# Kernel optimization log

Measured on AMD Instinct MI355X. Metric: run time of the kernel, lower is better.

Reference implementation:

```python
import jax, jax.numpy as jnp
import numpy as np

N = 100000
D_FEAT = 256
HID = 128
EMB = 64
FANOUT = 16


def setup_inputs() -> dict:
    key = jax.random.key(0)
    k = jax.random.split(key, 7)
    s = 0.05
    features = jax.random.normal(k[0], (N, D_FEAT), dtype=jnp.float32)
    W1 = jax.random.normal(k[1], (HID, 2 * D_FEAT), dtype=jnp.float32) * s
    W2 = jax.random.normal(k[2], (HID, 2 * HID), dtype=jnp.float32) * s
    W3 = jax.random.normal(k[3], (HID, 2 * HID), dtype=jnp.float32) * s
    W4 = jax.random.normal(k[4], (EMB, 2 * HID), dtype=jnp.float32) * s
    nodes = jnp.arange(N, dtype=jnp.int32)
    neigh = jax.random.randint(k[5], (N, FANOUT), 0, N, dtype=jnp.int32)
    return {"features": features, "W1": W1, "W2": W2, "W3": W3, "W4": W4,
            "nodes": nodes, "neigh": neigh}


def _sage_layer(h, neigh, W):
    # MeanAggregator: mean of sampled neighbor features  [N, d]
    neigh_mean = jnp.mean(h[neigh], axis=1)
    # Encoder (gcn=False): relu(W @ cat([self, neigh_mean]).T) -> [N, out]
    combined = jnp.concatenate([h, neigh_mean], axis=1)  # [N, 2d]
    return jax.nn.relu(combined @ W.T)


def reference(features, W1, W2, W3, W4, nodes, neigh):
    h1 = _sage_layer(features, neigh, W1)  # [N, HID]
    h2 = _sage_layer(h1, neigh, W2)        # [N, HID]
    h3 = _sage_layer(h2, neigh, W3)        # [N, HID]
    h4 = _sage_layer(h3, neigh, W4)        # [N, EMB]
    # GraphEmbeddingModule.forward returns gSAGE4(n).t() -> [len(n), EMB]
    return h4[nodes]
```

## Files before the change

### kernel.cpp

```cpp
#include <hip/hip_runtime.h>
#include <hip/hip_bf16.h>


constexpr int N_NODES = 100000;
constexpr int FANOUT  = 16;

typedef __attribute__((ext_vector_type(8))) short short8;
typedef __attribute__((ext_vector_type(4))) float f32x4;

__device__ inline unsigned short bf16_rne(float f) {
    unsigned u = __float_as_uint(f);
    return (unsigned short)((u + 0x7fffu + ((u >> 16) & 1u)) >> 16);
}
__device__ inline float bf16_tof(unsigned short s) {
    return __uint_as_float(((unsigned)s) << 16);
}

__global__ __launch_bounds__(256)
void prep_Bck(const float* __restrict__ W, unsigned short* __restrict__ Bhi,
              unsigned short* __restrict__ Blo, int D_IN, int D_OUT)
{
    int i = blockIdx.x * 256 + threadIdx.x;
    int total = 2 * D_OUT * D_IN;
    if (i >= total) return;
    int c = i / D_IN, k = i % D_IN;
    float v = (c < D_OUT) ? W[(size_t)c * (2 * D_IN) + k]
                          : W[(size_t)(c - D_OUT) * (2 * D_IN) + D_IN + k];
    unsigned short hi = bf16_rne(v);
    Bhi[i] = hi;
    Blo[i] = bf16_rne(v - bf16_tof(hi));
}

__global__ __launch_bounds__(256, 3)
void gemm1(const float* __restrict__ hf,
           const unsigned short* __restrict__ Bhi,
           const unsigned short* __restrict__ Blo,
           float* __restrict__ gs, unsigned short* __restrict__ gn, int N)
{
    constexpr int K = 256, C = 256, DO = 128, LDA = 40, LDB = 40;
    __shared__ unsigned short Ah[64 * LDA], Al[64 * LDA];
    __shared__ unsigned short Bh[C * LDB], Bl[C * LDB];

    const int tid  = threadIdx.x;
    const int wave = tid >> 6;
    const int lane = tid & 63;
    const int ml   = lane & 15;
    const int quad = lane >> 4;
    const int node0 = blockIdx.x * 64;

    f32x4 acc[4][4];
    #pragma unroll
    for (int mi = 0; mi < 4; ++mi)
        #pragma unroll
        for (int ni = 0; ni < 4; ++ni)
            acc[mi][ni] = (f32x4){0.f, 0.f, 0.f, 0.f};

    for (int k0 = 0; k0 < K; k0 += 32) {
        #pragma unroll
        for (int t = 0; t < 2; ++t) {
            int idx = tid + t * 256;
            int row = idx >> 3, c4 = idx & 7;
            int nd = node0 + row; if (nd >= N) nd = N - 1;
            float4 v = *(const float4*)&hf[(size_t)nd * K + k0 + c4 * 4];
            float vv[4] = {v.x, v.y, v.z, v.w};
            unsigned short hi[4], lo[4];
            #pragma unroll
            for (int e = 0; e < 4; ++e) {
                hi[e] = bf16_rne(vv[e]);
                lo[e] = bf16_rne(vv[e] - bf16_tof(hi[e]));
            }
            *(uint2*)&Ah[row * LDA + c4 * 4] = *(const uint2*)hi;
            *(uint2*)&Al[row * LDA + c4 * 4] = *(const uint2*)lo;
        }
        #pragma unroll
        for (int t = 0; t < 8; ++t) {
            int idx = tid + t * 256;
            int pl  = idx >> 10;
            int rem = idx & 1023;
            int row = rem >> 2, ch = rem & 3;
            const unsigned short* src = (pl ? Blo : Bhi) + (size_t)row * K + k0 + ch * 8;
            unsigned short* dst = (pl ? Bl : Bh) + row * LDB + ch * 8;
            *(uint4*)dst = *(const uint4*)src;
        }
        __syncthreads();

        short8 afh[4], afl[4];
        #pragma unroll
        for (int mi = 0; mi < 4; ++mi) {
            int r = mi * 16 + ml;
            afh[mi] = *(const short8*)&Ah[r * LDA + quad * 8];
            afl[mi] = *(const short8*)&Al[r * LDA + quad * 8];
        }
        #pragma unroll
        for (int ni = 0; ni < 4; ++ni) {
            int c = wave * 64 + ni * 16 + ml;
            short8 bh = *(const short8*)&Bh[c * LDB + quad * 8];
            short8 bl = *(const short8*)&Bl[c * LDB + quad * 8];
            #pragma unroll
            for (int mi = 0; mi < 4; ++mi) {
                acc[mi][ni] = __builtin_amdgcn_mfma_f32_16x16x32_bf16(afl[mi], bh, acc[mi][ni], 0, 0, 0);
                acc[mi][ni] = __builtin_amdgcn_mfma_f32_16x16x32_bf16(afh[mi], bl, acc[mi][ni], 0, 0, 0);
                acc[mi][ni] = __builtin_amdgcn_mfma_f32_16x16x32_bf16(afh[mi], bh, acc[mi][ni], 0, 0, 0);
            }
        }
        __syncthreads();
    }

    #pragma unroll
    for (int mi = 0; mi < 4; ++mi)
        #pragma unroll
        for (int r = 0; r < 4; ++r) {
            int node = node0 + mi * 16 + quad * 4 + r;
            if (node >= N) continue;
            #pragma unroll
            for (int ni = 0; ni < 4; ++ni) {
                int c = wave * 64 + ni * 16 + ml;
                float v = acc[mi][ni][r];
                if (c < DO) gs[(size_t)node * DO + c] = v;
                else        gn[(size_t)node * DO + (c - DO)] = bf16_rne(v);
            }
        }
}

template<int C>
__global__ __launch_bounds__(256, 2)
void fused_layer(const float* __restrict__ gs_in,
                 const unsigned short* __restrict__ gn_in,
                 const int* __restrict__ neigh,
                 const unsigned short* __restrict__ Bhi,
                 const unsigned short* __restrict__ Blo,
                 float* __restrict__ gs_out,
                 unsigned short* __restrict__ gn_out, int N)
{
    constexpr int K = 128, DO = C / 2, NI = C / 64, LDAF = 136, LDB = 40;
    __shared__ unsigned short Afh[64 * LDAF], Afl[64 * LDAF];
    __shared__ unsigned short Bh[C * LDB], Bl[C * LDB];

    const int tid  = threadIdx.x;
    const int wave = tid >> 6;
    const int lane = tid & 63;
    const int ml   = lane & 15;
    const int quad = lane >> 4;
    const int node0 = blockIdx.x * 64;

    {
        const int row = tid >> 2;
        const int seg = tid & 3;
        int nd = node0 + row; if (nd >= N) nd = N - 1;
        const int4* nb4 = (const int4*)(neigh + (size_t)nd * FANOUT);
        int4 q0 = nb4[0], q1 = nb4[1], q2 = nb4[2], q3 = nb4[3];
        int ids[FANOUT] = {q0.x, q0.y, q0.z, q0.w, q1.x, q1.y, q1.z, q1.w,
                           q2.x, q2.y, q2.z, q2.w, q3.x, q3.y, q3.z, q3.w};
        float acc[32];
        #pragma unroll
        for (int c = 0; c < 32; ++c) acc[c] = 0.f;
        #pragma unroll
        for (int j = 0; j < FANOUT; ++j) {
            const uint4* src = (const uint4*)&gn_in[(size_t)ids[j] * 128 + seg * 32];
            #pragma unroll
            for (int t = 0; t < 4; ++t) {
                uint4 q = src[t];
                acc[t*8+0] += __uint_as_float(q.x << 16);
                acc[t*8+1] += __uint_as_float(q.x & 0xffff0000u);
                acc[t*8+2] += __uint_as_float(q.y << 16);
                acc[t*8+3] += __uint_as_float(q.y & 0xffff0000u);
                acc[t*8+4] += __uint_as_float(q.z << 16);
                acc[t*8+5] += __uint_as_float(q.z & 0xffff0000u);
                acc[t*8+6] += __uint_as_float(q.w << 16);
                acc[t*8+7] += __uint_as_float(q.w & 0xffff0000u);
            }
        }
        const float inv = 1.0f / (float)FANOUT;
        alignas(16) unsigned short th[32], tl[32];
        const float4* gsp = (const float4*)&gs_in[(size_t)nd * 128 + seg * 32];
        #pragma unroll
        for (int t = 0; t < 8; ++t) {
            float4 s = gsp[t];
            float sv[4] = {s.x, s.y, s.z, s.w};
            #pragma unroll
            for (int e = 0; e < 4; ++e) {
                float h = fmaxf(fmaf(acc[t*4+e], inv, sv[e]), 0.f);
                unsigned short hi = bf16_rne(h);
                th[t*4+e] = hi;
                tl[t*4+e] = bf16_rne(h - bf16_tof(hi));
            }
        }
        #pragma unroll
        for (int t = 0; t < 4; ++t) {
            *(uint4*)&Afh[row * LDAF + seg * 32 + t * 8] = *(const uint4*)&th[t * 8];
            *(uint4*)&Afl[row * LDAF + seg * 32 + t * 8] = *(const uint4*)&tl[t * 8];
        }
    }

    f32x4 acc[4][NI];
    #pragma unroll
    for (int mi = 0; mi < 4; ++mi)
        #pragma unroll
        for (int ni = 0; ni < NI; ++ni)
            acc[mi][ni] = (f32x4){0.f, 0.f, 0.f, 0.f};

    for (int k0 = 0; k0 < K; k0 += 32) {
        constexpr int TOT = 2 * C * 4;
        #pragma unroll
        for (int t = 0; t < TOT / 256; ++t) {
            int idx = tid + t * 256;
            int pl  = idx / (C * 4);
            int rem = idx % (C * 4);
            int row = rem >> 2, ch = rem & 3;
            const unsigned short* src = (pl ? Blo : Bhi) + (size_t)row * K + k0 + ch * 8;
            unsigned short* dst = (pl ? Bl : Bh) + row * LDB + ch * 8;
            *(uint4*)dst = *(const uint4*)src;
        }
        __syncthreads();

        short8 afh[4], afl[4];
        #pragma unroll
        for (int mi = 0; mi < 4; ++mi) {
            int r = mi * 16 + ml;
            afh[mi] = *(const short8*)&Afh[r * LDAF + k0 + quad * 8];
            afl[mi] = *(const short8*)&Afl[r * LDAF + k0 + quad * 8];
        }
        #pragma unroll
        for (int ni = 0; ni < NI; ++ni) {
            int c = wave * (16 * NI) + ni * 16 + ml;
            short8 bh = *(const short8*)&Bh[c * LDB + quad * 8];
            short8 bl = *(const short8*)&Bl[c * LDB + quad * 8];
            #pragma unroll
            for (int mi = 0; mi < 4; ++mi) {
                acc[mi][ni] = __builtin_amdgcn_mfma_f32_16x16x32_bf16(afl[mi], bh, acc[mi][ni], 0, 0, 0);
                acc[mi][ni] = __builtin_amdgcn_mfma_f32_16x16x32_bf16(afh[mi], bl, acc[mi][ni], 0, 0, 0);
                acc[mi][ni] = __builtin_amdgcn_mfma_f32_16x16x32_bf16(afh[mi], bh, acc[mi][ni], 0, 0, 0);
            }
        }
        __syncthreads();
    }

    #pragma unroll
    for (int mi = 0; mi < 4; ++mi)
        #pragma unroll
        for (int r = 0; r < 4; ++r) {
            int node = node0 + mi * 16 + quad * 4 + r;
            if (node >= N) continue;
            #pragma unroll
            for (int ni = 0; ni < NI; ++ni) {
                int c = wave * (16 * NI) + ni * 16 + ml;
                float v = acc[mi][ni][r];
                if (c < DO) gs_out[(size_t)node * DO + c] = v;
                else        gn_out[(size_t)node * DO + (c - DO)] = bf16_rne(v);
            }
        }
}

__global__ __launch_bounds__(256)
void agg_out(const float* __restrict__ gs4, const unsigned short* __restrict__ gn4,
             const int* __restrict__ neigh, const int* __restrict__ nodes,
             float* __restrict__ out, int N)
{
    const int i    = blockIdx.x * 32 + (threadIdx.x >> 3);
    const int lane = threadIdx.x & 7;
    if (i >= N) return;
    const int nd = nodes[i];
    const int4* nb4 = (const int4*)(neigh + (size_t)nd * FANOUT);
    int4 q0 = nb4[0], q1 = nb4[1], q2 = nb4[2], q3 = nb4[3];
    int ids[FANOUT] = {q0.x, q0.y, q0.z, q0.w, q1.x, q1.y, q1.z, q1.w,
                       q2.x, q2.y, q2.z, q2.w, q3.x, q3.y, q3.z, q3.w};
    float acc[8];
    #pragma unroll
    for (int c = 0; c < 8; ++c) acc[c] = 0.f;
    #pragma unroll
    for (int j = 0; j < FANOUT; ++j) {
        uint4 q = *(const uint4*)&gn4[(size_t)ids[j] * 64 + lane * 8];
        acc[0] += __uint_as_float(q.x << 16);
        acc[1] += __uint_as_float(q.x & 0xffff0000u);
        acc[2] += __uint_as_float(q.y << 16);
        acc[3] += __uint_as_float(q.y & 0xffff0000u);
        acc[4] += __uint_as_float(q.z << 16);
        acc[5] += __uint_as_float(q.z & 0xffff0000u);
        acc[6] += __uint_as_float(q.w << 16);
        acc[7] += __uint_as_float(q.w & 0xffff0000u);
    }
    const float inv = 1.0f / (float)FANOUT;
    const float* s = gs4 + (size_t)nd * 64 + lane * 8;
    float4 s0 = *(const float4*)&s[0];
    float4 s1 = *(const float4*)&s[4];
    float4 o0, o1;
    o0.x = fmaxf(fmaf(acc[0], inv, s0.x), 0.f);
    o0.y = fmaxf(fmaf(acc[1], inv, s0.y), 0.f);
    o0.z = fmaxf(fmaf(acc[2], inv, s0.z), 0.f);
    o0.w = fmaxf(fmaf(acc[3], inv, s0.w), 0.f);
    o1.x = fmaxf(fmaf(acc[4], inv, s1.x), 0.f);
    o1.y = fmaxf(fmaf(acc[5], inv, s1.y), 0.f);
    o1.z = fmaxf(fmaf(acc[6], inv, s1.z), 0.f);
    o1.w = fmaxf(fmaf(acc[7], inv, s1.w), 0.f);
    float* op = out + (size_t)i * 64 + lane * 8;
    *(float4*)&op[0] = o0;
    *(float4*)&op[4] = o1;
}

extern "C" void kernel_launch(void* const* d_in, const int* in_sizes, int n_in,
                              void* d_out, int out_size, void* d_ws, size_t ws_size,
                              hipStream_t stream)
{
    const float* features = (const float*)d_in[0];
    const float* W1       = (const float*)d_in[1];
    const float* W2       = (const float*)d_in[2];
    const float* W3       = (const float*)d_in[3];
    const float* W4       = (const float*)d_in[4];
    const int*   nodes    = (const int*)d_in[5];
    const int*   neigh    = (const int*)d_in[6];
    float*       out      = (float*)d_out;

    unsigned short* B1h = (unsigned short*)d_ws;
    unsigned short* B1l = B1h + 65536;
    unsigned short* B2h = B1l + 65536;
    unsigned short* B2l = B2h + 32768;
    unsigned short* B3h = B2l + 32768;
    unsigned short* B3l = B3h + 32768;
    unsigned short* B4h = B3l + 32768;
    unsigned short* B4l = B4h + 16384;
    float* gs = (float*)(B4l + 16384);
    unsigned short* gnA = (unsigned short*)(gs + (size_t)N_NODES * 128);
    unsigned short* gnB = gnA + (size_t)N_NODES * 128;
    float* gs4 = (float*)gnB;
    unsigned short* gn4 = gnB + (size_t)N_NODES * 128;

    prep_Bck<<<(65536 + 255) / 256, 256, 0, stream>>>(W1, B1h, B1l, 256, 128);
    prep_Bck<<<(32768 + 255) / 256, 256, 0, stream>>>(W2, B2h, B2l, 128, 128);
    prep_Bck<<<(32768 + 255) / 256, 256, 0, stream>>>(W3, B3h, B3l, 128, 128);
    prep_Bck<<<(16384 + 255) / 256, 256, 0, stream>>>(W4, B4h, B4l, 128, 64);

    const int grid = (N_NODES + 63) / 64;

    gemm1<<<grid, 256, 0, stream>>>(features, B1h, B1l, gs, gnA, N_NODES);
    fused_layer<256><<<grid, 256, 0, stream>>>(gs, gnA, neigh, B2h, B2l, gs, gnB, N_NODES);
    fused_layer<256><<<grid, 256, 0, stream>>>(gs, gnB, neigh, B3h, B3l, gs, gnA, N_NODES);
    fused_layer<128><<<grid, 256, 0, stream>>>(gs, gnA, neigh, B4h, B4l, gs4, gn4, N_NODES);
    agg_out<<<(N_NODES + 31) / 32, 256, 0, stream>>>(gs4, gn4, neigh, nodes, out, N_NODES);
}
```

Baseline: 509.0 us.

## Read weight fragments directly from global memory instead of staging in LDS

Drops the per-k-step copy of the split bf16 weight matrices into shared memory in both the first GEMM and the fused layer kernels. Each wave now loads its B fragments straight from global memory, which should hit L2 cache because the weights are small. Per-iteration barriers in the fused layer go away, and the smaller LDS footprint allows the occupancy hint to rise to 4 blocks per CU. The cost is more uncached-per-wave global loads with higher latency in the MFMA inner loop, and register pressure under the tighter launch bound.

```diff
diff --git a/kernel.cpp b/kernel.cpp
--- a/kernel.cpp
+++ b/kernel.cpp
@@ -31,15 +31,14 @@
     Blo[i] = bf16_rne(v - bf16_tof(hi));
 }
 
-__global__ __launch_bounds__(256, 3)
+__global__ __launch_bounds__(256, 4)
 void gemm1(const float* __restrict__ hf,
            const unsigned short* __restrict__ Bhi,
            const unsigned short* __restrict__ Blo,
            float* __restrict__ gs, unsigned short* __restrict__ gn, int N)
 {
-    constexpr int K = 256, C = 256, DO = 128, LDA = 40, LDB = 40;
+    constexpr int K = 256, DO = 128, LDA = 40;
     __shared__ unsigned short Ah[64 * LDA], Al[64 * LDA];
-    __shared__ unsigned short Bh[C * LDB], Bl[C * LDB];
 
     const int tid  = threadIdx.x;
     const int wave = tid >> 6;
@@ -72,16 +71,6 @@
             *(uint2*)&Ah[row * LDA + c4 * 4] = *(const uint2*)hi;
             *(uint2*)&Al[row * LDA + c4 * 4] = *(const uint2*)lo;
         }
-        #pragma unroll
-        for (int t = 0; t < 8; ++t) {
-            int idx = tid + t * 256;
-            int pl  = idx >> 10;
-            int rem = idx & 1023;
-            int row = rem >> 2, ch = rem & 3;
-            const unsigned short* src = (pl ? Blo : Bhi) + (size_t)row * K + k0 + ch * 8;
-            unsigned short* dst = (pl ? Bl : Bh) + row * LDB + ch * 8;
-            *(uint4*)dst = *(const uint4*)src;
-        }
         __syncthreads();
 
         short8 afh[4], afl[4];
@@ -94,8 +83,8 @@
         #pragma unroll
         for (int ni = 0; ni < 4; ++ni) {
             int c = wave * 64 + ni * 16 + ml;
-            short8 bh = *(const short8*)&Bh[c * LDB + quad * 8];
-            short8 bl = *(const short8*)&Bl[c * LDB + quad * 8];
+            short8 bh = *(const short8*)&Bhi[(size_t)c * K + k0 + quad * 8];
+            short8 bl = *(const short8*)&Blo[(size_t)c * K + k0 + quad * 8];
             #pragma unroll
             for (int mi = 0; mi < 4; ++mi) {
                 acc[mi][ni] = __builtin_amdgcn_mfma_f32_16x16x32_bf16(afl[mi], bh, acc[mi][ni], 0, 0, 0);
@@ -123,7 +112,7 @@
 }
 
 template<int C>
-__global__ __launch_bounds__(256, 2)
+__global__ __launch_bounds__(256, 4)
 void fused_layer(const float* __restrict__ gs_in,
                  const unsigned short* __restrict__ gn_in,
                  const int* __restrict__ neigh,
@@ -132,9 +121,8 @@
                  float* __restrict__ gs_out,
                  unsigned short* __restrict__ gn_out, int N)
 {
-    constexpr int K = 128, DO = C / 2, NI = C / 64, LDAF = 136, LDB = 40;
+    constexpr int K = 128, DO = C / 2, NI = C / 64, LDAF = 136;
     __shared__ unsigned short Afh[64 * LDAF], Afl[64 * LDAF];
-    __shared__ unsigned short Bh[C * LDB], Bl[C * LDB];
 
     const int tid  = threadIdx.x;
     const int wave = tid >> 6;
@@ -191,6 +179,7 @@
             *(uint4*)&Afl[row * LDAF + seg * 32 + t * 8] = *(const uint4*)&tl[t * 8];
         }
     }
+    __syncthreads();
 
     f32x4 acc[4][NI];
     #pragma unroll
@@ -200,19 +189,6 @@
             acc[mi][ni] = (f32x4){0.f, 0.f, 0.f, 0.f};
 
     for (int k0 = 0; k0 < K; k0 += 32) {
-        constexpr int TOT = 2 * C * 4;
-        #pragma unroll
-        for (int t = 0; t < TOT / 256; ++t) {
-            int idx = tid + t * 256;
-            int pl  = idx / (C * 4);
-            int rem = idx % (C * 4);
-            int row = rem >> 2, ch = rem & 3;
-            const unsigned short* src = (pl ? Blo : Bhi) + (size_t)row * K + k0 + ch * 8;
-            unsigned short* dst = (pl ? Bl : Bh) + row * LDB + ch * 8;
-            *(uint4*)dst = *(const uint4*)src;
-        }
-        __syncthreads();
-
         short8 afh[4], afl[4];
         #pragma unroll
         for (int mi = 0; mi < 4; ++mi) {
@@ -223,8 +199,8 @@
         #pragma unroll
         for (int ni = 0; ni < NI; ++ni) {
             int c = wave * (16 * NI) + ni * 16 + ml;
-            short8 bh = *(const short8*)&Bh[c * LDB + quad * 8];
-            short8 bl = *(const short8*)&Bl[c * LDB + quad * 8];
+            short8 bh = *(const short8*)&Bhi[(size_t)c * K + k0 + quad * 8];
+            short8 bl = *(const short8*)&Blo[(size_t)c * K + k0 + quad * 8];
             #pragma unroll
             for (int mi = 0; mi < 4; ++mi) {
                 acc[mi][ni] = __builtin_amdgcn_mfma_f32_16x16x32_bf16(afl[mi], bh, acc[mi][ni], 0, 0, 0);
@@ -232,7 +208,6 @@
                 acc[mi][ni] = __builtin_amdgcn_mfma_f32_16x16x32_bf16(afh[mi], bh, acc[mi][ni], 0, 0, 0);
             }
         }
-        __syncthreads();
     }
 
     #pragma unroll
```

Result: slower. 537.6 us (+5.6%).
